# Kernel tuning notes

Hardware: AMD Instinct MI355X
Metric: run time of the kernel (lower is better)

## Reference

```python
import jax, jax.numpy as jnp
import numpy as np

B, D, H, W, K = 32, 128, 128, 128, 32

def setup_inputs() -> dict:
    key = jax.random.key(0)
    k1, k2, k3 = jax.random.split(key, 3)
    X = jax.random.normal(k1, (B, D, H, W), dtype=jnp.float32)
    std1 = 1.0 / np.sqrt(K * D)
    codewords = jax.random.uniform(k2, (K, D), dtype=jnp.float32, minval=-std1, maxval=std1)
    scale = jax.random.uniform(k3, (K,), dtype=jnp.float32, minval=-1.0, maxval=0.0)
    return {"X": X, "codewords": codewords, "scale": scale}

def reference(X, codewords, scale):
    # X: [B, D, H, W] -> [B, N, D]
    b, d = X.shape[0], X.shape[1]
    x = X.reshape(b, d, -1).transpose(0, 2, 1)  # [B, N, D]
    x2 = jnp.sum(x * x, axis=-1, keepdims=True)            # [B, N, 1]
    c2 = jnp.sum(codewords * codewords, axis=-1)           # [K]
    xc = jnp.einsum('bnd,kd->bnk', x, codewords)           # [B, N, K]
    sl = scale * (x2 - 2.0 * xc + c2)                      # [B, N, K]
    A = jax.nn.softmax(sl, axis=2)                         # assignment weights
    # E[b,k,d] = sum_n A[b,n,k] * (x[b,n,d] - c[k,d])
    E = jnp.einsum('bnk,bnd->bkd', A, x) - jnp.sum(A, axis=1)[..., None] * codewords
    return E
```

## Files before the change

### kernel.cpp

```cpp
#include <hip/hip_runtime.h>
#include <hip/hip_bf16.h>

#define B_   32
#define D_   128
#define N_   16384
#define K_   32
#define NS   256
#define AST_STRIDE 264

#define WS_WBF  0
#define WS_SC   2048
#define WS_C2S  2080
#define WS_EP   2112

typedef __attribute__((ext_vector_type(8))) short bf16x8;
typedef __attribute__((ext_vector_type(4))) float f32x4;

static __device__ inline unsigned int pk2(float lo, float hi) {
    __hip_bfloat162 h = __float22bfloat162_rn(make_float2(lo, hi));
    unsigned int r;
    __builtin_memcpy(&r, &h, 4);
    return r;
}

static __device__ inline bf16x8 pack8(const float* v) {
    union { unsigned int u[4]; bf16x8 f; } r;
    r.u[0] = pk2(v[0], v[1]);
    r.u[1] = pk2(v[2], v[3]);
    r.u[2] = pk2(v[4], v[5]);
    r.u[3] = pk2(v[6], v[7]);
    return r.f;
}

__global__ void prep_kernel(const float* __restrict__ cw,
                            const float* __restrict__ scale,
                            float* __restrict__ ws) {
    const int k = blockIdx.x;
    const int l = threadIdx.x;
    const float sc = scale[k] * 1.44269504088896f;
    unsigned short* Wbf = (unsigned short*)(ws + WS_WBF);
    float s = 0.f;
#pragma unroll
    for (int i = 0; i < 2; ++i) {
        const int d = l + i * 64;
        const float v = cw[k * D_ + d];
        s += v * v;
        const float w = -2.f * sc * v;
        unsigned int u = __float_as_uint(w);
        u += 0x7fffu + ((u >> 16) & 1u);
        Wbf[k * D_ + d] = (unsigned short)(u >> 16);
    }
#pragma unroll
    for (int o = 32; o > 0; o >>= 1) s += __shfl_down(s, o, 64);
    if (l == 0) {
        ws[WS_SC  + k] = sc;
        ws[WS_C2S + k] = sc * s;
    }
}

template<int NCHUNKT>
__global__ __launch_bounds__(256, 6) void main_kernel(
        const float* __restrict__ X,
        const float* __restrict__ ws_ro,
        float* __restrict__ AsumP,
        float* __restrict__ Ep)
{
    constexpr int CSZT  = N_ / NCHUNKT;
    constexpr int NSUBT = CSZT / NS;

    __shared__ __align__(16) unsigned short AsT[K_ * AST_STRIDE];

    const int t    = threadIdx.x;
    const int lane = t & 63;
    const int w    = t >> 6;
    const int mc   = lane & 15;
    const int q    = lane >> 4;

    const int blk   = blockIdx.x;
    const int b     = blk / NCHUNKT;
    const int chunk = blk % NCHUNKT;
    const int n0    = chunk * CSZT;

    const float* Xb = X + (size_t)b * ((size_t)D_ * N_);

    const unsigned short* Wbf = (const unsigned short*)(ws_ro + WS_WBF);
    bf16x8 wf[2][4];
#pragma unroll
    for (int kb = 0; kb < 2; ++kb)
#pragma unroll
        for (int kd = 0; kd < 4; ++kd)
            wf[kb][kd] = *(const bf16x8*)&Wbf[(kb * 16 + mc) * D_ + kd * 32 + q * 8];

    float scr[2][4], c2r[2][4];
#pragma unroll
    for (int kb = 0; kb < 2; ++kb)
#pragma unroll
        for (int r = 0; r < 4; ++r) {
            scr[kb][r] = ws_ro[WS_SC  + kb * 16 + q * 4 + r];
            c2r[kb][r] = ws_ro[WS_C2S + kb * 16 + q * 4 + r];
        }

    bf16x8 ones;
#pragma unroll
    for (int i = 0; i < 8; ++i) ones[i] = (short)0x3F80;

    f32x4 accE[2][2] = {{{0.f,0.f,0.f,0.f},{0.f,0.f,0.f,0.f}},
                        {{0.f,0.f,0.f,0.f},{0.f,0.f,0.f,0.f}}};
    f32x4 accO[2]    = {{0.f,0.f,0.f,0.f},{0.f,0.f,0.f,0.f}};

    for (int s = 0; s < NSUBT; ++s) {
        const int ns = n0 + s * NS;

#pragma unroll 1
        for (int cb = 0; cb < 4; ++cb) {
            const int ntl = (w * 4 + cb) * 16;
            const float* xp = Xb + ns + ntl + mc;

            f32x4 S0 = {0.f,0.f,0.f,0.f};
            f32x4 S1 = {0.f,0.f,0.f,0.f};
            float x2 = 0.f;
#pragma unroll
            for (int kdp = 0; kdp < 2; ++kdp) {
                float xv[16];
#pragma unroll
                for (int h = 0; h < 2; ++h)
#pragma unroll
                    for (int j = 0; j < 8; ++j)
                        xv[h * 8 + j] =
                            xp[(size_t)((kdp * 2 + h) * 32 + q * 8 + j) * N_];
#pragma unroll
                for (int i = 0; i < 16; ++i) x2 = fmaf(xv[i], xv[i], x2);
#pragma unroll
                for (int h = 0; h < 2; ++h) {
                    const bf16x8 xb = pack8(&xv[h * 8]);
                    const int kd = kdp * 2 + h;
                    S0 = __builtin_amdgcn_mfma_f32_16x16x32_bf16(wf[0][kd], xb, S0, 0, 0, 0);
                    S1 = __builtin_amdgcn_mfma_f32_16x16x32_bf16(wf[1][kd], xb, S1, 0, 0, 0);
                }
            }
            x2 += __shfl_xor(x2, 16, 64);
            x2 += __shfl_xor(x2, 32, 64);

            float sl[8];
#pragma unroll
            for (int r = 0; r < 4; ++r) {
                sl[r]     = fmaf(scr[0][r], x2, S0[r] + c2r[0][r]);
                sl[4 + r] = fmaf(scr[1][r], x2, S1[r] + c2r[1][r]);
            }
            float m = sl[0];
#pragma unroll
            for (int i = 1; i < 8; ++i) m = fmaxf(m, sl[i]);
            m = fmaxf(m, __shfl_xor(m, 16, 64));
            m = fmaxf(m, __shfl_xor(m, 32, 64));
            float ssum = 0.f;
#pragma unroll
            for (int i = 0; i < 8; ++i) { sl[i] = exp2f(sl[i] - m); ssum += sl[i]; }
            ssum += __shfl_xor(ssum, 16, 64);
            ssum += __shfl_xor(ssum, 32, 64);
            const float inv = 1.f / ssum;

            const int col = ntl + mc;
#pragma unroll
            for (int r = 0; r < 4; ++r) {
                const unsigned int u = pk2(sl[r] * inv, sl[4 + r] * inv);
                AsT[(q * 4 + r) * AST_STRIDE + col]        = (unsigned short)u;
                AsT[(16 + q * 4 + r) * AST_STRIDE + col]   = (unsigned short)(u >> 16);
            }
        }
        __syncthreads();

        const int dq = w;
#pragma unroll 2
        for (int ks = 0; ks < NS / 32; ++ks) {
            const int nl = ks * 32 + q * 8;
            const bf16x8 a0 = *(const bf16x8*)&AsT[mc * AST_STRIDE + nl];
            const bf16x8 a1 = *(const bf16x8*)&AsT[(16 + mc) * AST_STRIDE + nl];

            const float* bp = Xb + (size_t)(dq * 32 + mc) * N_ + ns + nl;
            float xr[8];
            *(float4*)&xr[0] = *(const float4*)bp;
            *(float4*)&xr[4] = *(const float4*)(bp + 4);
            const bf16x8 xb0 = pack8(xr);
            const float* bp2 = bp + (size_t)16 * N_;
            float xs[8];
            *(float4*)&xs[0] = *(const float4*)bp2;
            *(float4*)&xs[4] = *(const float4*)(bp2 + 4);
            const bf16x8 xb1 = pack8(xs);

            accE[0][0] = __builtin_amdgcn_mfma_f32_16x16x32_bf16(a0, xb0, accE[0][0], 0, 0, 0);
            accE[0][1] = __builtin_amdgcn_mfma_f32_16x16x32_bf16(a0, xb1, accE[0][1], 0, 0, 0);
            accE[1][0] = __builtin_amdgcn_mfma_f32_16x16x32_bf16(a1, xb0, accE[1][0], 0, 0, 0);
            accE[1][1] = __builtin_amdgcn_mfma_f32_16x16x32_bf16(a1, xb1, accE[1][1], 0, 0, 0);
            if (w == 0) {
                accO[0] = __builtin_amdgcn_mfma_f32_16x16x32_bf16(a0, ones, accO[0], 0, 0, 0);
                accO[1] = __builtin_amdgcn_mfma_f32_16x16x32_bf16(a1, ones, accO[1], 0, 0, 0);
            }
        }
        __syncthreads();
    }

    float* EpB = Ep + (size_t)blk * (K_ * D_);
#pragma unroll
    for (int kh = 0; kh < 2; ++kh)
#pragma unroll
        for (int ds = 0; ds < 2; ++ds)
#pragma unroll
            for (int r = 0; r < 4; ++r) {
                const int k = kh * 16 + q * 4 + r;
                const int d = w * 32 + ds * 16 + mc;
                EpB[k * D_ + d] = accE[kh][ds][r];
            }
    if (w == 0 && mc == 0) {
#pragma unroll
        for (int kh = 0; kh < 2; ++kh)
#pragma unroll
            for (int r = 0; r < 4; ++r)
                AsumP[blk * K_ + kh * 16 + q * 4 + r] = accO[kh][r];
    }
}

template<int NCHUNKT>
__global__ void finalize_kernel(const float* __restrict__ cw,
                                const float* __restrict__ AsumP,
                                const float* __restrict__ Ep,
                                float* __restrict__ out)
{
    const int idx = blockIdx.x * 256 + threadIdx.x;
    const int d = idx & 127;
    const int k = (idx >> 7) & 31;
    const int b = idx >> 12;
    float s = 0.f, asum = 0.f;
#pragma unroll 8
    for (int c = 0; c < NCHUNKT; ++c) {
        const int blk = b * NCHUNKT + c;
        s    += Ep[(size_t)blk * (K_ * D_) + k * D_ + d];
        asum += AsumP[blk * K_ + k];
    }
    out[idx] = s - asum * cw[k * D_ + d];
}

extern "C" void kernel_launch(void* const* d_in, const int* in_sizes, int n_in,
                              void* d_out, int out_size, void* d_ws, size_t ws_size,
                              hipStream_t stream) {
    const float* X     = (const float*)d_in[0];
    const float* cw    = (const float*)d_in[1];
    const float* scale = (const float*)d_in[2];
    float* out = (float*)d_out;
    float* ws  = (float*)d_ws;

    prep_kernel<<<K_, 64, 0, stream>>>(cw, scale, ws);

    const size_t need64 = (size_t)(WS_EP + 2048 * (K_ * D_ + K_)) * 4;
    const size_t need32 = (size_t)(WS_EP + 1024 * (K_ * D_ + K_)) * 4;
    if (ws_size >= need64) {
        float* Ep    = ws + WS_EP;
        float* AsumP = Ep + (size_t)2048 * (K_ * D_);
        main_kernel<64><<<B_ * 64, 256, 0, stream>>>(X, ws, AsumP, Ep);
        finalize_kernel<64><<<(B_ * K_ * D_) / 256, 256, 0, stream>>>(cw, AsumP, Ep, out);
    } else if (ws_size >= need32) {
        float* Ep    = ws + WS_EP;
        float* AsumP = Ep + (size_t)1024 * (K_ * D_);
        main_kernel<32><<<B_ * 32, 256, 0, stream>>>(X, ws, AsumP, Ep);
        finalize_kernel<32><<<(B_ * K_ * D_) / 256, 256, 0, stream>>>(cw, AsumP, Ep, out);
    } else {
        float* Ep    = ws + WS_EP;
        float* AsumP = Ep + (size_t)512 * (K_ * D_);
        main_kernel<16><<<B_ * 16, 256, 0, stream>>>(X, ws, AsumP, Ep);
        finalize_kernel<16><<<(B_ * K_ * D_) / 256, 256, 0, stream>>>(cw, AsumP, Ep, out);
    }
}
```

Before: 427.4 us.

## Stage X tile in swizzled LDS as bf16 and prefetch next sub-tile

X is now read from global memory once per sub-tile. It is converted to bf16 and written into a swizzled shared-memory tile, so the second (A^T·X) GEMM reads operands from LDS instead of reloading X from global. Loads for the next sub-tile are issued into registers right after the barrier, overlapping them with the E-accumulation MFMAs. The sub-tile shrinks from 256 to 128 points and occupancy bounds drop from 6 to 3 waves per SIMD, trading higher register and LDS use for less global traffic.

```diff
diff --git a/kernel.cpp b/kernel.cpp
--- a/kernel.cpp
+++ b/kernel.cpp
@@ -5,8 +5,9 @@
 #define D_   128
 #define N_   16384
 #define K_   32
-#define NS   256
-#define AST_STRIDE 264
+#define NS   128
+#define XST  136
+#define ASTS 136
 
 #define WS_WBF  0
 #define WS_SC   2048
@@ -59,7 +60,7 @@
 }
 
 template<int NCHUNKT>
-__global__ __launch_bounds__(256, 6) void main_kernel(
+__global__ __launch_bounds__(256, 3) void main_kernel(
         const float* __restrict__ X,
         const float* __restrict__ ws_ro,
         float* __restrict__ AsumP,
@@ -68,7 +69,8 @@
     constexpr int CSZT  = N_ / NCHUNKT;
     constexpr int NSUBT = CSZT / NS;
 
-    __shared__ __align__(16) unsigned short AsT[K_ * AST_STRIDE];
+    __shared__ __align__(16) unsigned short Xs[D_ * XST];
+    __shared__ __align__(16) unsigned short AsT[K_ * ASTS];
 
     const int t    = threadIdx.x;
     const int lane = t & 63;
@@ -108,39 +110,57 @@
                         {{0.f,0.f,0.f,0.f},{0.f,0.f,0.f,0.f}}};
     f32x4 accO[2]    = {{0.f,0.f,0.f,0.f},{0.f,0.f,0.f,0.f}};
 
+    float xv[2][2][16];
+    auto load_sub = [&](int ssub) {
+        const int nsb = n0 + ssub * NS;
+#pragma unroll
+        for (int cb = 0; cb < 2; ++cb) {
+            const float* xp = Xb + nsb + w * 32 + cb * 16 + mc;
+#pragma unroll
+            for (int kdp = 0; kdp < 2; ++kdp)
+#pragma unroll
+                for (int i = 0; i < 16; ++i) {
+                    const int h = i >> 3, j = i & 7;
+                    xv[cb][kdp][i] = xp[(size_t)((kdp * 2 + h) * 32 + q * 8 + j) * N_];
+                }
+        }
+    };
+
+    load_sub(0);
+
     for (int s = 0; s < NSUBT; ++s) {
-        const int ns = n0 + s * NS;
-
-#pragma unroll 1
-        for (int cb = 0; cb < 4; ++cb) {
-            const int ntl = (w * 4 + cb) * 16;
-            const float* xp = Xb + ns + ntl + mc;
-
+#pragma unroll
+        for (int cb = 0; cb < 2; ++cb) {
+            const int col = w * 32 + cb * 16 + mc;
             f32x4 S0 = {0.f,0.f,0.f,0.f};
             f32x4 S1 = {0.f,0.f,0.f,0.f};
             float x2 = 0.f;
+            bf16x8 xbf[4];
 #pragma unroll
             for (int kdp = 0; kdp < 2; ++kdp) {
-                float xv[16];
-#pragma unroll
-                for (int h = 0; h < 2; ++h)
-#pragma unroll
-                    for (int j = 0; j < 8; ++j)
-                        xv[h * 8 + j] =
-                            xp[(size_t)((kdp * 2 + h) * 32 + q * 8 + j) * N_];
-#pragma unroll
-                for (int i = 0; i < 16; ++i) x2 = fmaf(xv[i], xv[i], x2);
-#pragma unroll
-                for (int h = 0; h < 2; ++h) {
-                    const bf16x8 xb = pack8(&xv[h * 8]);
-                    const int kd = kdp * 2 + h;
-                    S0 = __builtin_amdgcn_mfma_f32_16x16x32_bf16(wf[0][kd], xb, S0, 0, 0, 0);
-                    S1 = __builtin_amdgcn_mfma_f32_16x16x32_bf16(wf[1][kd], xb, S1, 0, 0, 0);
+#pragma unroll
+                for (int i = 0; i < 16; ++i)
+                    x2 = fmaf(xv[cb][kdp][i], xv[cb][kdp][i], x2);
+                xbf[kdp * 2]     = pack8(&xv[cb][kdp][0]);
+                xbf[kdp * 2 + 1] = pack8(&xv[cb][kdp][8]);
+#pragma unroll
+                for (int h2 = 0; h2 < 2; ++h2) {
+                    const int kd = kdp * 2 + h2;
+                    S0 = __builtin_amdgcn_mfma_f32_16x16x32_bf16(wf[0][kd], xbf[kd], S0, 0, 0, 0);
+                    S1 = __builtin_amdgcn_mfma_f32_16x16x32_bf16(wf[1][kd], xbf[kd], S1, 0, 0, 0);
                 }
             }
+
+            const int baseW = ((((col >> 3) ^ (q << 1)) << 3) + (col & 7));
+#pragma unroll
+            for (int kd = 0; kd < 4; ++kd)
+#pragma unroll
+                for (int jj = 0; jj < 8; ++jj)
+                    Xs[(kd * 32 + q * 8 + jj) * XST + baseW] =
+                        ((const unsigned short*)&xbf[kd])[jj];
+
             x2 += __shfl_xor(x2, 16, 64);
             x2 += __shfl_xor(x2, 32, 64);
-
             float sl[8];
 #pragma unroll
             for (int r = 0; r < 4; ++r) {
@@ -158,39 +178,34 @@
             ssum += __shfl_xor(ssum, 16, 64);
             ssum += __shfl_xor(ssum, 32, 64);
             const float inv = 1.f / ssum;
-
-            const int col = ntl + mc;
 #pragma unroll
             for (int r = 0; r < 4; ++r) {
                 const unsigned int u = pk2(sl[r] * inv, sl[4 + r] * inv);
-                AsT[(q * 4 + r) * AST_STRIDE + col]        = (unsigned short)u;
-                AsT[(16 + q * 4 + r) * AST_STRIDE + col]   = (unsigned short)(u >> 16);
+                AsT[(q * 4 + r) * ASTS + col]      = (unsigned short)u;
+                AsT[(16 + q * 4 + r) * ASTS + col] = (unsigned short)(u >> 16);
             }
         }
         __syncthreads();
 
-        const int dq = w;
-#pragma unroll 2
+        if (s + 1 < NSUBT) load_sub(s + 1);
+
+#pragma unroll
         for (int ks = 0; ks < NS / 32; ++ks) {
             const int nl = ks * 32 + q * 8;
-            const bf16x8 a0 = *(const bf16x8*)&AsT[mc * AST_STRIDE + nl];
-            const bf16x8 a1 = *(const bf16x8*)&AsT[(16 + mc) * AST_STRIDE + nl];
-
-            const float* bp = Xb + (size_t)(dq * 32 + mc) * N_ + ns + nl;
-            float xr[8];
-            *(float4*)&xr[0] = *(const float4*)bp;
-            *(float4*)&xr[4] = *(const float4*)(bp + 4);
-            const bf16x8 xb0 = pack8(xr);
-            const float* bp2 = bp + (size_t)16 * N_;
-            float xs[8];
-            *(float4*)&xs[0] = *(const float4*)bp2;
-            *(float4*)&xs[4] = *(const float4*)(bp2 + 4);
-            const bf16x8 xb1 = pack8(xs);
-
-            accE[0][0] = __builtin_amdgcn_mfma_f32_16x16x32_bf16(a0, xb0, accE[0][0], 0, 0, 0);
-            accE[0][1] = __builtin_amdgcn_mfma_f32_16x16x32_bf16(a0, xb1, accE[0][1], 0, 0, 0);
-            accE[1][0] = __builtin_amdgcn_mfma_f32_16x16x32_bf16(a1, xb0, accE[1][0], 0, 0, 0);
-            accE[1][1] = __builtin_amdgcn_mfma_f32_16x16x32_bf16(a1, xb1, accE[1][1], 0, 0, 0);
+            const bf16x8 a0 = *(const bf16x8*)&AsT[mc * ASTS + nl];
+            const bf16x8 a1 = *(const bf16x8*)&AsT[(16 + mc) * ASTS + nl];
+
+            bf16x8 xb[2];
+#pragma unroll
+            for (int ds = 0; ds < 2; ++ds) {
+                const int su = (ks * 4 + q) ^ ((((ds * 2) + (mc >> 3)) & 3) << 1);
+                xb[ds] = *(const bf16x8*)&Xs[(w * 32 + ds * 16 + mc) * XST + su * 8];
+            }
+
+            accE[0][0] = __builtin_amdgcn_mfma_f32_16x16x32_bf16(a0, xb[0], accE[0][0], 0, 0, 0);
+            accE[0][1] = __builtin_amdgcn_mfma_f32_16x16x32_bf16(a0, xb[1], accE[0][1], 0, 0, 0);
+            accE[1][0] = __builtin_amdgcn_mfma_f32_16x16x32_bf16(a1, xb[0], accE[1][0], 0, 0, 0);
+            accE[1][1] = __builtin_amdgcn_mfma_f32_16x16x32_bf16(a1, xb[1], accE[1][1], 0, 0, 0);
             if (w == 0) {
                 accO[0] = __builtin_amdgcn_mfma_f32_16x16x32_bf16(a0, ones, accO[0], 0, 0, 0);
                 accO[1] = __builtin_amdgcn_mfma_f32_16x16x32_bf16(a1, ones, accO[1], 0, 0, 0);
```

New measurement: 668.2 us. 56.3% more time.
